# Kernel optimization log

Measured on AMD Instinct MI355X. Metric: run time of the kernel, lower is better.

The kernel has to match this reference:

```python
import jax, jax.numpy as jnp
import numpy as np

# dims
N = 10000      # nodes
E = 320000     # edges (avg degree 32)
NS = 64        # hidden 0e scalar channels
NV = 64        # hidden 1o vector channels
EMB = 32       # node-attr embedding dim
NTYPES = 20    # max_atom_types
NB = 8         # number_of_basis (bessel)
RH = 16        # radial_neurons
L = 2          # layers
CUT = 3.5      # max_radius
NNEIGH = 32.0  # num_neighbors normalization
H = 0.1        # residual step size


def smooth_cutoff(u):
    # e3nn example smooth_cutoff applied to x/max_radius
    v = 2.0 * (u - 1.0)
    y = 0.5 * (1.0 - jnp.cos(jnp.pi * v))
    y = jnp.where(v > 0.0, 0.0, y)
    y = jnp.where(v < -1.0, 1.0, y)
    return y


def setup_inputs() -> dict:
    key = jax.random.key(0)
    ks = jax.random.split(key, 10)
    x = jax.random.normal(ks[0], (N, 6), jnp.float32)
    batch = jnp.zeros((N,), jnp.int32)
    node_attr = jax.random.randint(ks[1], (N,), 0, NTYPES)
    edge_src = jax.random.randint(ks[2], (E,), 0, N)
    # avoid self-loops (zero edge length -> NaN in sh / bessel)
    off = jax.random.randint(ks[3], (E,), 1, N)
    edge_dst = (edge_src + off) % N
    embed_table = 0.1 * jax.random.normal(ks[4], (NTYPES, EMB), jnp.float32)
    Ku = jax.random.normal(ks[5], (2, NV), jnp.float32)          # uplift (made semi-unitary via QR)
    W_sc_s = 0.05 * jax.random.normal(ks[6], (L, NS, EMB, NS + NV), jnp.float32)  # self-connection TP: scalars
    W_sc_v = 0.05 * jax.random.normal(ks[7], (L, NV, EMB, NV), jnp.float32)       # self-connection TP: vectors
    Wr1 = 0.3 * jax.random.normal(ks[8], (L, NB, RH), jnp.float32)
    br1 = jnp.zeros((L, RH), jnp.float32)
    Wr2 = 0.3 * jax.random.normal(ks[9], (L, RH, 4 * NV), jnp.float32)
    br2 = jnp.zeros((L, 4 * NV), jnp.float32)
    return {"x": x, "batch": batch, "node_attr": node_attr, "edge_src": edge_src,
            "edge_dst": edge_dst, "embed_table": embed_table, "Ku": Ku,
            "W_sc_s": W_sc_s, "W_sc_v": W_sc_v, "Wr1": Wr1, "br1": br1,
            "Wr2": Wr2, "br2": br2}


def reference(x, batch, node_attr, edge_src, edge_dst, embed_table, Ku,
              W_sc_s, W_sc_v, Wr1, br1, Wr2, br2):
    n = x.shape[0]
    a = embed_table[node_attr]                     # [n, EMB] node-attr embedding (0e scalars)
    # make uplift semi-unitary: Q^T Q = I_2
    Q, _ = jnp.linalg.qr(Ku.T)                     # [NV, 2]
    U = Q.T                                        # uplift [2, NV]
    x_v = x.reshape(n, 2, 3)                       # 2x1o: position, velocity
    y_s = jnp.zeros((n, NS), x.dtype)              # uplift has no 1o->0e path
    y_v = jnp.einsum('ncd,ch->nhd', x_v, U)        # [n, NV, 3]
    nfreq = jnp.arange(1, NB + 1, dtype=x.dtype)
    inv_deg = 1.0 / np.sqrt(NNEIGH)
    for l in range(L):
        pos = x_v[:, 0, :]
        ev = pos[edge_src] - pos[edge_dst]                          # [E, 3]
        elen = jnp.linalg.norm(ev, axis=1)                          # [E]
        sh = jnp.sqrt(3.0) * ev / elen[:, None]                     # 1x1o SH, component norm
        # bessel radial basis, scaled by sqrt(NB)
        bess = (jnp.sqrt(2.0 / CUT) * jnp.sin(jnp.pi * nfreq * elen[:, None] / CUT)
                / elen[:, None]) * np.sqrt(NB)                      # [E, NB]
        ea = smooth_cutoff(elen / CUT)[:, None] * sh                # edge_attr [E, 3]
        # radial MLP -> per-edge tensor-product weights (4 paths x NV channels)
        w = jax.nn.silu(bess @ Wr1[l] + br1[l]) @ Wr2[l] + br2[l]   # [E, 4*NV]
        wA, wB, wC, wD = jnp.split(w, 4, axis=1)
        s_src = y_s[edge_src]                                       # [E, NS]
        v_src = y_v[edge_src]                                       # [E, NV, 3]
        # TP paths: 0e x 1o -> 1o ; 1o x 1o -> 1o (cross) ; 1o x 1o -> 0e (dot, feats + gates)
        msg_v = (wA[:, :, None] * s_src[:, :, None] * ea[:, None, :]
                 + wC[:, :, None] * jnp.cross(v_src, ea[:, None, :]))  # [E, NV, 3]
        dots = jnp.einsum('evd,ed->ev', v_src, ea)                  # [E, NV]
        msg_s = jnp.concatenate([wB * dots, wD * dots], axis=1)     # [E, NS+NV]
        agg_s = jax.ops.segment_sum(msg_s, edge_dst, num_segments=n) * inv_deg
        agg_v = (jax.ops.segment_sum(msg_v.reshape(msg_v.shape[0], -1), edge_dst,
                                     num_segments=n).reshape(n, NV, 3) * inv_deg)
        # self-connection: fully-connected TP with node-attr scalars
        sc_s = jnp.einsum('ns,ne,seo->no', y_s, a, W_sc_s[l])       # [n, NS+NV]
        sc_v = jnp.einsum('nvd,ne,veu->nud', y_v, a, W_sc_v[l])     # [n, NV, 3]
        out_s = sc_s + agg_s
        out_v = sc_v + agg_v
        # gate: silu on scalar feats, sigmoid gates scale the vectors
        y_s = y_s + H * jax.nn.silu(out_s[:, :NS])
        y_v = y_v + H * jax.nn.sigmoid(out_s[:, NS:])[:, :, None] * out_v
        # project back to 2x1o
        x_v = jnp.einsum('nhd,hc->ncd', y_v, Q)
    return x_v.reshape(n, 6)
```

## Files before the change

### kernel.cpp

```cpp
#include <hip/hip_runtime.h>
#include <math.h>

#define NSC 64
#define NVC 64
#define EMB 32
#define NTYPES 20
#define NB 8
#define RH 16
#define LAYERS 2
#define CUTV 3.5f
#define HSTEP 0.1f

__device__ __forceinline__ float wave_sum(float t)
{
  #pragma unroll
  for (int mm = 1; mm < 64; mm <<= 1) t += __shfl_xor(t, mm, 64);
  return t;
}

__global__ void qr_kernel(const float* __restrict__ Ku, float* __restrict__ Q)
{
  const int i = threadIdx.x;
  float a0 = Ku[i], a1 = Ku[64 + i];
  const float xn2 = wave_sum((i >= 1) ? a0 * a0 : 0.f);
  const float alpha = __shfl(a0, 0, 64);
  const float beta0 = -copysignf(sqrtf(alpha * alpha + xn2), alpha);
  const float tau0 = (beta0 - alpha) / beta0;
  const float inv0 = 1.f / (alpha - beta0);
  const float v0 = (i == 0) ? 1.f : a0 * inv0;
  const float w = wave_sum(v0 * a1);
  a1 -= tau0 * w * v0;
  const float alpha1 = __shfl(a1, 1, 64);
  const float xn2b = wave_sum((i >= 2) ? a1 * a1 : 0.f);
  const float beta1 = -copysignf(sqrtf(alpha1 * alpha1 + xn2b), alpha1);
  const float tau1 = (beta1 - alpha1) / beta1;
  const float inv1 = 1.f / (alpha1 - beta1);
  const float v1 = (i == 0) ? 0.f : ((i == 1) ? 1.f : a1 * inv1);
  const float t1v = ((i == 1) ? 1.f : 0.f) - tau1 * v1;
  const float d = wave_sum(v0 * t1v);
  Q[i * 2 + 0] = ((i == 0) ? 1.f : 0.f) - tau0 * v0;
  Q[i * 2 + 1] = t1v - tau0 * d * v0;
}

__global__ void init_state(const float* __restrict__ x, const float* __restrict__ Qm,
                           float4* __restrict__ st0, int* __restrict__ cnt, int n)
{
  const int i = blockIdx.x * 256 + threadIdx.x;
  const int node = i >> 6, lane = i & 63;
  if (node < n) {
    const float q0 = Qm[lane * 2 + 0], q1 = Qm[lane * 2 + 1];
    const float* xp = x + (size_t)node * 6;
    st0[i] = make_float4(0.f,
                         xp[0] * q0 + xp[3] * q1,
                         xp[1] * q0 + xp[4] * q1,
                         xp[2] * q0 + xp[5] * q1);
  }
  if (i < n) cnt[i] = 0;
}

__global__ void hist_kernel(const int* __restrict__ edst, int* __restrict__ cnt, int m)
{
  const int e = blockIdx.x * 256 + threadIdx.x;
  if (e < m) atomicAdd(&cnt[edst[e]], 1);
}

__global__ void scan_kernel(int* cnt, int* off, int n)
{
  __shared__ int lds[1024];
  const int t = threadIdx.x;
  const int CH = (n + 1023) >> 10;
  const int base = t * CH;
  int local[16];
  int run = 0;
  for (int j = 0; j < CH; ++j) {
    int v = (base + j < n) ? cnt[base + j] : 0;
    local[j] = run;
    run += v;
  }
  lds[t] = run;
  __syncthreads();
  for (int s = 1; s < 1024; s <<= 1) {
    int v = (t >= s) ? lds[t - s] : 0;
    __syncthreads();
    lds[t] += v;
    __syncthreads();
  }
  const int excl = lds[t] - run;
  for (int j = 0; j < CH; ++j) {
    if (base + j < n) {
      int o = excl + local[j];
      off[base + j] = o;
      cnt[base + j] = o;
    }
  }
  if (t == 1023) off[n] = lds[1023];
}

__global__ void scatter_kernel(const int* __restrict__ esrc, const int* __restrict__ edst,
                               int* __restrict__ cursor,
                               int* __restrict__ esrc_s, int* __restrict__ edst_s, int m)
{
  const int e = blockIdx.x * 256 + threadIdx.x;
  if (e < m) {
    const int d = edst[e];
    int p = atomicAdd(&cursor[d], 1);
    esrc_s[p] = esrc[e];
    edst_s[p] = d;
  }
}

__global__ void type_weights(const float* __restrict__ embed,
                             const float* __restrict__ Wss,
                             const float* __restrict__ Wsv,
                             float* __restrict__ Ws, float* __restrict__ Wv,
                             int total_s, int total_v)
{
  const int i = blockIdx.x * 256 + threadIdx.x;
  if (i < total_s) {
    const int bid = i >> 13;
    const int p = i & 8191;
    const int l = bid / NTYPES, t = bid % NTYPES;
    const int s = p >> 7, o = p & 127;
    const float* ar = embed + t * EMB;
    const float* wp = Wss + ((size_t)(l * 64 + s) * EMB) * 128 + o;
    float acc = 0.f;
    #pragma unroll
    for (int e = 0; e < EMB; ++e) acc = fmaf(ar[e], wp[e * 128], acc);
    Ws[i] = acc;
  } else {
    const int j = i - total_s;
    if (j < total_v) {
      const int bid = j >> 12;
      const int p = j & 4095;
      const int l = bid / NTYPES, t = bid % NTYPES;
      const int v = p >> 6, u = p & 63;
      const float* ar = embed + t * EMB;
      const float* wp = Wsv + ((size_t)(l * 64 + v) * EMB) * 64 + u;
      float acc = 0.f;
      #pragma unroll
      for (int e = 0; e < EMB; ++e) acc = fmaf(ar[e], wp[e * 64], acc);
      Wv[j] = acc;
    }
  }
}

__global__ void transpose_wr2(const float* __restrict__ Wr2, float* __restrict__ Wt)
{
  const int t = blockIdx.x * 256 + threadIdx.x;
  if (t >= LAYERS * 256) return;
  const int l = t >> 8, ch = t & 255;
  #pragma unroll
  for (int j = 0; j < RH; ++j)
    Wt[(size_t)l * 4096 + ch * RH + j] = Wr2[(size_t)l * 4096 + j * 256 + ch];
}

__global__ void edge_geom(const float* __restrict__ xv,
                          const int* __restrict__ esrc_s, const int* __restrict__ edst_s,
                          const float* __restrict__ Wr1l, const float* __restrict__ br1l,
                          float4* __restrict__ ea4, float* __restrict__ hidb, int m)
{
  const int k = blockIdx.x * 256 + threadIdx.x;
  if (k >= m) return;
  const int s = esrc_s[k], d = edst_s[k];
  const float ex = xv[(size_t)s * 6 + 0] - xv[(size_t)d * 6 + 0];
  const float ey = xv[(size_t)s * 6 + 1] - xv[(size_t)d * 6 + 1];
  const float ez = xv[(size_t)s * 6 + 2] - xv[(size_t)d * 6 + 2];
  const float len = sqrtf(ex * ex + ey * ey + ez * ez);
  const float invl = 1.f / len;
  const float u = len * (1.f / CUTV);
  const float arg = (float)M_PI * u;
  float sa, ca;
  __sincosf(arg, &sa, &ca);
  const float vv = 2.f * (u - 1.f);
  float cut = 0.5f * (1.f - (2.f * ca * ca - 1.f));
  cut = (vv > 0.f) ? 0.f : cut;
  cut = (vv < -1.f) ? 1.f : cut;
  const float cc = cut * 1.7320508075688772f * invl;
  ea4[k] = make_float4(cc * ex, cc * ey, cc * ez, 0.f);
  float bess[NB];
  const float amp = 2.1380899352993948f * invl;
  const float twoc = 2.f * ca;
  float sm1 = 0.f, scur = sa;
  #pragma unroll
  for (int kk = 0; kk < NB; ++kk) {
    bess[kk] = amp * scur;
    const float snext = twoc * scur - sm1;
    sm1 = scur; scur = snext;
  }
  float hid[RH];
  #pragma unroll
  for (int j = 0; j < RH; ++j) {
    float h = br1l[j];
    #pragma unroll
    for (int kk = 0; kk < NB; ++kk) h = fmaf(bess[kk], Wr1l[kk * RH + j], h);
    hid[j] = h / (1.f + expf(-h));
  }
  float4* hp = (float4*)(hidb + (size_t)k * 16);
  hp[0] = make_float4(hid[0],  hid[1],  hid[2],  hid[3]);
  hp[1] = make_float4(hid[4],  hid[5],  hid[6],  hid[7]);
  hp[2] = make_float4(hid[8],  hid[9],  hid[10], hid[11]);
  hp[3] = make_float4(hid[12], hid[13], hid[14], hid[15]);
}

#define MLPW                                                                  \
  float w = bias;                                                             \
  w = fmaf(g1.x, W0.x, w); w = fmaf(g1.y, W0.y, w);                           \
  w = fmaf(g1.z, W0.z, w); w = fmaf(g1.w, W0.w, w);                           \
  w = fmaf(g2.x, W1.x, w); w = fmaf(g2.y, W1.y, w);                           \
  w = fmaf(g2.z, W1.z, w); w = fmaf(g2.w, W1.w, w);                           \
  w = fmaf(g3.x, W2.x, w); w = fmaf(g3.y, W2.y, w);                           \
  w = fmaf(g3.z, W2.z, w); w = fmaf(g3.w, W2.w, w);                           \
  w = fmaf(g4.x, W3.x, w); w = fmaf(g4.y, W3.y, w);                           \
  w = fmaf(g4.z, W3.z, w); w = fmaf(g4.w, W3.w, w);

#define EDGE_PIPELINE(QSTMT)                                                  \
  {                                                                           \
    int k = k0;                                                               \
    for (; k + 4 <= k1; k += 4) {                                             \
      const int sA = esrc_s[k],     sB = esrc_s[k + 1];                       \
      const int sC = esrc_s[k + 2], sD = esrc_s[k + 3];                       \
      const float4 stA = st_in[(size_t)sA * 64 + lane];                       \
      const float4 stB = st_in[(size_t)sB * 64 + lane];                       \
      const float4 stC = st_in[(size_t)sC * 64 + lane];                       \
      const float4 stD = st_in[(size_t)sD * 64 + lane];                       \
      const float4 eaA = ea4[k],     eaB = ea4[k + 1];                        \
      const float4 eaC = ea4[k + 2], eaD = ea4[k + 3];                        \
      const float4* hb = (const float4*)(hidb + (size_t)k * 16);              \
      { const float4 g1 = hb[0], g2 = hb[1], g3 = hb[2], g4 = hb[3];          \
        const float4 stc = stA, ea = eaA; MLPW; QSTMT }                       \
      { const float4 g1 = hb[4], g2 = hb[5], g3 = hb[6], g4 = hb[7];          \
        const float4 stc = stB, ea = eaB; MLPW; QSTMT }                       \
      { const float4 g1 = hb[8], g2 = hb[9], g3 = hb[10], g4 = hb[11];        \
        const float4 stc = stC, ea = eaC; MLPW; QSTMT }                       \
      { const float4 g1 = hb[12], g2 = hb[13], g3 = hb[14], g4 = hb[15];      \
        const float4 stc = stD, ea = eaD; MLPW; QSTMT }                       \
    }                                                                         \
    for (; k < k1; ++k) {                                                     \
      const int sA = esrc_s[k];                                               \
      const float4 stc = st_in[(size_t)sA * 64 + lane];                       \
      const float4* hb = (const float4*)(hidb + (size_t)k * 16);              \
      const float4 g1 = hb[0], g2 = hb[1], g3 = hb[2], g4 = hb[3];            \
      const float4 ea = ea4[k];                                               \
      MLPW; QSTMT                                                             \
    }                                                                         \
  }

__global__ __launch_bounds__(256, 3) void gather_update(
    const int* __restrict__ off, const int* __restrict__ esrc_s,
    const float4* __restrict__ ea4, const float* __restrict__ hidb,
    const float4* __restrict__ st_in, const int* __restrict__ nattr,
    const float* __restrict__ Ws, const float* __restrict__ Wv,
    const float* __restrict__ Wtl, const float* __restrict__ br2l,
    const float* __restrict__ Qm,
    float4* __restrict__ st_out, float* __restrict__ xv_out, int n)
{
  __shared__ float eAx[64], eAy[64], eAz[64], eCx[64], eCy[64], eCz[64];
  __shared__ float eB[64], eD[64];
  __shared__ float oP[4][5][64];
  const int lane = threadIdx.x & 63;
  const int wid = threadIdx.x >> 6;
  const int node = blockIdx.x;

  const int chg = (wid << 6) + lane;
  const float* wp = Wtl + (size_t)chg * RH;
  const float4 W0 = *(const float4*)wp;
  const float4 W1 = *(const float4*)(wp + 4);
  const float4 W2 = *(const float4*)(wp + 8);
  const float4 W3 = *(const float4*)(wp + 12);
  const float bias = br2l[chg];

  float a0 = 0.f, a1 = 0.f, a2 = 0.f;
  const int k0 = off[node], k1 = off[node + 1];
  if (k0 < k1) {
    if (wid == 0) {
      EDGE_PIPELINE({
        const float t = w * stc.x;
        a0 = fmaf(t, ea.x, a0); a1 = fmaf(t, ea.y, a1); a2 = fmaf(t, ea.z, a2);
      })
    } else if (wid == 1) {
      EDGE_PIPELINE({
        const float dt = stc.y * ea.x + stc.z * ea.y + stc.w * ea.z;
        a0 = fmaf(w, dt, a0);
      })
    } else if (wid == 2) {
      EDGE_PIPELINE({
        a0 = fmaf(w, stc.z * ea.z - stc.w * ea.y, a0);
        a1 = fmaf(w, stc.w * ea.x - stc.y * ea.z, a1);
        a2 = fmaf(w, stc.y * ea.y - stc.z * ea.x, a2);
      })
    } else {
      EDGE_PIPELINE({
        const float dt = stc.y * ea.x + stc.z * ea.y + stc.w * ea.z;
        a0 = fmaf(w, dt, a0);
      })
    }
  }
  if (wid == 0)      { eAx[lane] = a0; eAy[lane] = a1; eAz[lane] = a2; }
  else if (wid == 1) { eB[lane] = a0; }
  else if (wid == 2) { eCx[lane] = a0; eCy[lane] = a1; eCz[lane] = a2; }
  else               { eD[lane] = a0; }

  const int ty = nattr[node];
  const float* WsT = Ws + (size_t)ty * 8192;
  const float* WvT = Wv + (size_t)ty * 4096;
  const float4 own = st_in[(size_t)node * 64 + lane];
  float oS1 = 0.f, oS2 = 0.f, oV0 = 0.f, oV1 = 0.f, oV2 = 0.f;
  const int s20 = wid << 4;
  #pragma unroll 4
  for (int s2 = s20; s2 < s20 + 16; ++s2) {
    const float yss = __shfl(own.x, s2, 64);
    const float b0 = __shfl(own.y, s2, 64);
    const float b1 = __shfl(own.z, s2, 64);
    const float b2 = __shfl(own.w, s2, 64);
    oS1 = fmaf(yss, WsT[s2 * 128 + lane], oS1);
    oS2 = fmaf(yss, WsT[s2 * 128 + 64 + lane], oS2);
    const float wvv = WvT[s2 * 64 + lane];
    oV0 = fmaf(b0, wvv, oV0);
    oV1 = fmaf(b1, wvv, oV1);
    oV2 = fmaf(b2, wvv, oV2);
  }
  oP[wid][0][lane] = oS1; oP[wid][1][lane] = oS2;
  oP[wid][2][lane] = oV0; oP[wid][3][lane] = oV1; oP[wid][4][lane] = oV2;
  __syncthreads();

  if (wid == 0) {
    const float inv_deg = 0.17677669529663687f;
    const float aS1 = eB[lane], aS2 = eD[lane];
    const float aV0 = eAx[lane] + eCx[lane];
    const float aV1 = eAy[lane] + eCy[lane];
    const float aV2 = eAz[lane] + eCz[lane];
    float s1 = 0.f, s2v = 0.f, v0 = 0.f, v1 = 0.f, v2 = 0.f;
    #pragma unroll
    for (int q = 0; q < 4; ++q) {
      s1 += oP[q][0][lane]; s2v += oP[q][1][lane];
      v0 += oP[q][2][lane]; v1 += oP[q][3][lane]; v2 += oP[q][4][lane];
    }
    const float outS1 = s1 + aS1 * inv_deg;
    const float outS2 = s2v + aS2 * inv_deg;
    const float sig1 = 1.f / (1.f + expf(-outS1));
    const float gate = 1.f / (1.f + expf(-outS2));
    const float ysn = own.x + HSTEP * outS1 * sig1;
    const float gf = HSTEP * gate;
    const float yvn0 = own.y + gf * (v0 + aV0 * inv_deg);
    const float yvn1 = own.z + gf * (v1 + aV1 * inv_deg);
    const float yvn2 = own.w + gf * (v2 + aV2 * inv_deg);
    st_out[(size_t)node * 64 + lane] = make_float4(ysn, yvn0, yvn1, yvn2);

    const float q0 = Qm[lane * 2 + 0], q1 = Qm[lane * 2 + 1];
    float pr[6] = { yvn0 * q0, yvn1 * q0, yvn2 * q0,
                    yvn0 * q1, yvn1 * q1, yvn2 * q1 };
    #pragma unroll
    for (int mm = 1; mm < 64; mm <<= 1) {
      #pragma unroll
      for (int i = 0; i < 6; ++i) pr[i] += __shfl_xor(pr[i], mm, 64);
    }
    if (lane == 0) {
      #pragma unroll
      for (int i = 0; i < 6; ++i) xv_out[(size_t)node * 6 + i] = pr[i];
    }
  }
}

extern "C" void kernel_launch(void* const* d_in, const int* in_sizes, int n_in,
                              void* d_out, int out_size, void* d_ws, size_t ws_size,
                              hipStream_t stream)
{
  const float* x     = (const float*)d_in[0];
  const int*   nattr = (const int*)d_in[2];
  const int*   esrc  = (const int*)d_in[3];
  const int*   edst  = (const int*)d_in[4];
  const float* embed = (const float*)d_in[5];
  const float* Ku    = (const float*)d_in[6];
  const float* Wss   = (const float*)d_in[7];
  const float* Wsv   = (const float*)d_in[8];
  const float* Wr1   = (const float*)d_in[9];
  const float* br1   = (const float*)d_in[10];
  const float* Wr2   = (const float*)d_in[11];
  const float* br2   = (const float*)d_in[12];
  const int n = in_sizes[0] / 6;
  const int m = in_sizes[3];

  char* p = (char*)d_ws;
  auto alloc = [&](size_t bytes) -> char* {
    char* r = p;
    p += (bytes + 255) & ~(size_t)255;
    return r;
  };
  int*    off    = (int*)alloc((size_t)(n + 1) * 4);
  int*    cursor = (int*)alloc((size_t)n * 4);
  int*    esrc_s = (int*)alloc((size_t)m * 4);
  int*    edst_s = (int*)alloc((size_t)m * 4);
  float*  Q      = (float*)alloc(128 * 4);
  float*  Ws     = (float*)alloc((size_t)LAYERS * NTYPES * 64 * 128 * 4);
  float*  Wv     = (float*)alloc((size_t)LAYERS * NTYPES * 64 * 64 * 4);
  float4* st0    = (float4*)alloc((size_t)n * 64 * 16);
  float4* st1    = (float4*)alloc((size_t)n * 64 * 16);
  float*  xvb    = (float*)alloc((size_t)n * 6 * 4);
  float4* ea4    = (float4*)alloc((size_t)m * 16);
  float*  hidb   = (float*)alloc((size_t)m * 16 * 4);
  float*  Wt     = (float*)alloc((size_t)LAYERS * 4096 * 4);

  const int total_s = LAYERS * NTYPES * 64 * 128;
  const int total_v = LAYERS * NTYPES * 64 * 64;

  qr_kernel<<<1, 64, 0, stream>>>(Ku, Q);
  init_state<<<(n * 64 + 255) / 256, 256, 0, stream>>>(x, Q, st0, cursor, n);
  hist_kernel<<<(m + 255) / 256, 256, 0, stream>>>(edst, cursor, m);
  scan_kernel<<<1, 1024, 0, stream>>>(cursor, off, n);
  scatter_kernel<<<(m + 255) / 256, 256, 0, stream>>>(esrc, edst, cursor, esrc_s, edst_s, m);
  type_weights<<<(total_s + total_v + 255) / 256, 256, 0, stream>>>(
      embed, Wss, Wsv, Ws, Wv, total_s, total_v);
  transpose_wr2<<<2, 256, 0, stream>>>(Wr2, Wt);

  const float* xv_cur = x;
  const float4* st_cur = st0;
  float4* st_nxt = st1;
  for (int l = 0; l < LAYERS; ++l) {
    edge_geom<<<(m + 255) / 256, 256, 0, stream>>>(
        xv_cur, esrc_s, edst_s, Wr1 + l * NB * RH, br1 + l * RH, ea4, hidb, m);
    float* xv_out = (l == LAYERS - 1) ? (float*)d_out : xvb;
    gather_update<<<n, 256, 0, stream>>>(
        off, esrc_s, ea4, hidb, st_cur, nattr,
        Ws + (size_t)l * NTYPES * 8192, Wv + (size_t)l * NTYPES * 4096,
        Wt + (size_t)l * 4096, br2 + l * 256, Q,
        st_nxt, xv_out, n);
    xv_cur = xv_out;
    float4* ts = (float4*)st_cur; st_cur = st_nxt; st_nxt = ts;
  }
}
```

Baseline: 305.4 us.

## Share gathered source rows across waves via double-buffered LDS staging

Each of the four waves used to gather every neighbour's 1 KB source-node row from global memory on its own. Now each wave loads two of every eight edges into a double-buffered shared-memory stage, and all waves read from it. The next batch's loads are issued before the current batch is consumed. This cuts redundant global gathers by roughly fourfold, at the cost of 16 KB more LDS per block (possibly lower occupancy), a block-wide barrier per 8-edge batch, and masked padding work on partial batches.

```diff
diff --git a/kernel.cpp b/kernel.cpp
--- a/kernel.cpp
+++ b/kernel.cpp
@@ -213,36 +213,19 @@
   w = fmaf(g4.x, W3.x, w); w = fmaf(g4.y, W3.y, w);                           \
   w = fmaf(g4.z, W3.z, w); w = fmaf(g4.w, W3.w, w);
 
-#define EDGE_PIPELINE(QSTMT)                                                  \
-  {                                                                           \
-    int k = k0;                                                               \
-    for (; k + 4 <= k1; k += 4) {                                             \
-      const int sA = esrc_s[k],     sB = esrc_s[k + 1];                       \
-      const int sC = esrc_s[k + 2], sD = esrc_s[k + 3];                       \
-      const float4 stA = st_in[(size_t)sA * 64 + lane];                       \
-      const float4 stB = st_in[(size_t)sB * 64 + lane];                       \
-      const float4 stC = st_in[(size_t)sC * 64 + lane];                       \
-      const float4 stD = st_in[(size_t)sD * 64 + lane];                       \
-      const float4 eaA = ea4[k],     eaB = ea4[k + 1];                        \
-      const float4 eaC = ea4[k + 2], eaD = ea4[k + 3];                        \
-      const float4* hb = (const float4*)(hidb + (size_t)k * 16);              \
-      { const float4 g1 = hb[0], g2 = hb[1], g3 = hb[2], g4 = hb[3];          \
-        const float4 stc = stA, ea = eaA; MLPW; QSTMT }                       \
-      { const float4 g1 = hb[4], g2 = hb[5], g3 = hb[6], g4 = hb[7];          \
-        const float4 stc = stB, ea = eaB; MLPW; QSTMT }                       \
-      { const float4 g1 = hb[8], g2 = hb[9], g3 = hb[10], g4 = hb[11];        \
-        const float4 stc = stC, ea = eaC; MLPW; QSTMT }                       \
-      { const float4 g1 = hb[12], g2 = hb[13], g3 = hb[14], g4 = hb[15];      \
-        const float4 stc = stD, ea = eaD; MLPW; QSTMT }                       \
-    }                                                                         \
-    for (; k < k1; ++k) {                                                     \
-      const int sA = esrc_s[k];                                               \
-      const float4 stc = st_in[(size_t)sA * 64 + lane];                       \
-      const float4* hb = (const float4*)(hidb + (size_t)k * 16);              \
-      const float4 g1 = hb[0], g2 = hb[1], g3 = hb[2], g4 = hb[3];            \
-      const float4 ea = ea4[k];                                               \
-      MLPW; QSTMT                                                             \
-    }                                                                         \
+#define CONSUME(QSTMT)                                                        \
+  _Pragma("unroll")                                                           \
+  for (int e = 0; e < 8; ++e) {                                               \
+    const int kk = kb + e;                                                    \
+    const int idx = (kk < k1) ? kk : (k1 - 1);                                \
+    const float mval = (kk < k1) ? 1.f : 0.f;                                 \
+    const float4 stc = stg[cur][e][lane];                                     \
+    const float4* hb = (const float4*)(hidb + (size_t)idx * 16);              \
+    const float4 g1 = hb[0], g2 = hb[1], g3 = hb[2], g4 = hb[3];              \
+    const float4 ea = ea4[idx];                                               \
+    MLPW;                                                                     \
+    w *= mval;                                                                \
+    QSTMT                                                                     \
   }
 
 __global__ __launch_bounds__(256, 3) void gather_update(
@@ -254,6 +237,7 @@
     const float* __restrict__ Qm,
     float4* __restrict__ st_out, float* __restrict__ xv_out, int n)
 {
+  __shared__ float4 stg[2][8][64];
   __shared__ float eAx[64], eAy[64], eAz[64], eCx[64], eCy[64], eCz[64];
   __shared__ float eB[64], eD[64];
   __shared__ float oP[4][5][64];
@@ -272,27 +256,57 @@
   float a0 = 0.f, a1 = 0.f, a2 = 0.f;
   const int k0 = off[node], k1 = off[node + 1];
   if (k0 < k1) {
-    if (wid == 0) {
-      EDGE_PIPELINE({
-        const float t = w * stc.x;
-        a0 = fmaf(t, ea.x, a0); a1 = fmaf(t, ea.y, a1); a2 = fmaf(t, ea.z, a2);
-      })
-    } else if (wid == 1) {
-      EDGE_PIPELINE({
-        const float dt = stc.y * ea.x + stc.z * ea.y + stc.w * ea.z;
-        a0 = fmaf(w, dt, a0);
-      })
-    } else if (wid == 2) {
-      EDGE_PIPELINE({
-        a0 = fmaf(w, stc.z * ea.z - stc.w * ea.y, a0);
-        a1 = fmaf(w, stc.w * ea.x - stc.y * ea.z, a1);
-        a2 = fmaf(w, stc.y * ea.y - stc.z * ea.x, a2);
-      })
-    } else {
-      EDGE_PIPELINE({
-        const float dt = stc.y * ea.x + stc.z * ea.y + stc.w * ea.z;
-        a0 = fmaf(w, dt, a0);
-      })
+    const int nb = (k1 - k0 + 7) >> 3;
+    {
+      const int i0 = k0 + wid, i1 = k0 + 4 + wid;
+      const int s0 = esrc_s[(i0 < k1) ? i0 : (k1 - 1)];
+      const int s1 = esrc_s[(i1 < k1) ? i1 : (k1 - 1)];
+      const float4 r0 = st_in[(size_t)s0 * 64 + lane];
+      const float4 r1 = st_in[(size_t)s1 * 64 + lane];
+      stg[0][wid][lane] = r0;
+      stg[0][wid + 4][lane] = r1;
+    }
+    __syncthreads();
+    for (int b = 0; b < nb; ++b) {
+      const int kb = k0 + (b << 3);
+      const int cur = b & 1, nxt = cur ^ 1;
+      float4 r0, r1;
+      const bool have_next = (b + 1 < nb);
+      if (have_next) {
+        const int kn = kb + 8;
+        const int i0 = kn + wid, i1 = kn + 4 + wid;
+        const int s0 = esrc_s[(i0 < k1) ? i0 : (k1 - 1)];
+        const int s1 = esrc_s[(i1 < k1) ? i1 : (k1 - 1)];
+        r0 = st_in[(size_t)s0 * 64 + lane];
+        r1 = st_in[(size_t)s1 * 64 + lane];
+      }
+      if (wid == 0) {
+        CONSUME({
+          const float t = w * stc.x;
+          a0 = fmaf(t, ea.x, a0); a1 = fmaf(t, ea.y, a1); a2 = fmaf(t, ea.z, a2);
+        })
+      } else if (wid == 1) {
+        CONSUME({
+          const float dt = stc.y * ea.x + stc.z * ea.y + stc.w * ea.z;
+          a0 = fmaf(w, dt, a0);
+        })
+      } else if (wid == 2) {
+        CONSUME({
+          a0 = fmaf(w, stc.z * ea.z - stc.w * ea.y, a0);
+          a1 = fmaf(w, stc.w * ea.x - stc.y * ea.z, a1);
+          a2 = fmaf(w, stc.y * ea.y - stc.z * ea.x, a2);
+        })
+      } else {
+        CONSUME({
+          const float dt = stc.y * ea.x + stc.z * ea.y + stc.w * ea.z;
+          a0 = fmaf(w, dt, a0);
+        })
+      }
+      if (have_next) {
+        stg[nxt][wid][lane] = r0;
+        stg[nxt][wid + 4][lane] = r1;
+      }
+      __syncthreads();
     }
   }
   if (wid == 0)      { eAx[lane] = a0; eAy[lane] = a1; eAz[lane] = a2; }
```

Measured after the change: 383.2 us. +25.5%, slower.

## Store node state in bf16 and gather 8 edges per masked batch

Applied to the files above, without the earlier changes.

Node state (scalar plus vector channels) is now stored as bf16 ushort4 instead of float4, which halves the bytes of the random per-edge gathers of source-node state in gather_update. The edge loop now fetches 8 edges per iteration with clamped indices and a zero mask on padded slots, replacing the 4-wide loop plus scalar tail, to keep more loads in flight. The cost is reduced precision in the state carried between layers, extra register pressure, and wasted work on padded edges.

```diff
diff --git a/kernel.cpp b/kernel.cpp
--- a/kernel.cpp
+++ b/kernel.cpp
@@ -10,6 +10,17 @@
 #define LAYERS 2
 #define CUTV 3.5f
 #define HSTEP 0.1f
+
+__device__ __forceinline__ unsigned short f2bf(float f)
+{
+  unsigned u = __float_as_uint(f);
+  unsigned r = (u + 0x7FFFu + ((u >> 16) & 1u)) >> 16;
+  return (unsigned short)r;
+}
+__device__ __forceinline__ float bf2f(unsigned short u)
+{
+  return __uint_as_float(((unsigned)u) << 16);
+}
 
 __device__ __forceinline__ float wave_sum(float t)
 {
@@ -43,17 +54,17 @@
 }
 
 __global__ void init_state(const float* __restrict__ x, const float* __restrict__ Qm,
-                           float4* __restrict__ st0, int* __restrict__ cnt, int n)
+                           ushort4* __restrict__ st0, int* __restrict__ cnt, int n)
 {
   const int i = blockIdx.x * 256 + threadIdx.x;
   const int node = i >> 6, lane = i & 63;
   if (node < n) {
     const float q0 = Qm[lane * 2 + 0], q1 = Qm[lane * 2 + 1];
     const float* xp = x + (size_t)node * 6;
-    st0[i] = make_float4(0.f,
-                         xp[0] * q0 + xp[3] * q1,
-                         xp[1] * q0 + xp[4] * q1,
-                         xp[2] * q0 + xp[5] * q1);
+    st0[i] = make_ushort4(0,
+                          f2bf(xp[0] * q0 + xp[3] * q1),
+                          f2bf(xp[1] * q0 + xp[4] * q1),
+                          f2bf(xp[2] * q0 + xp[5] * q1));
   }
   if (i < n) cnt[i] = 0;
 }
@@ -214,45 +225,42 @@
   w = fmaf(g4.z, W3.z, w); w = fmaf(g4.w, W3.w, w);
 
 #define EDGE_PIPELINE(QSTMT)                                                  \
-  {                                                                           \
-    int k = k0;                                                               \
-    for (; k + 4 <= k1; k += 4) {                                             \
-      const int sA = esrc_s[k],     sB = esrc_s[k + 1];                       \
-      const int sC = esrc_s[k + 2], sD = esrc_s[k + 3];                       \
-      const float4 stA = st_in[(size_t)sA * 64 + lane];                       \
-      const float4 stB = st_in[(size_t)sB * 64 + lane];                       \
-      const float4 stC = st_in[(size_t)sC * 64 + lane];                       \
-      const float4 stD = st_in[(size_t)sD * 64 + lane];                       \
-      const float4 eaA = ea4[k],     eaB = ea4[k + 1];                        \
-      const float4 eaC = ea4[k + 2], eaD = ea4[k + 3];                        \
-      const float4* hb = (const float4*)(hidb + (size_t)k * 16);              \
-      { const float4 g1 = hb[0], g2 = hb[1], g3 = hb[2], g4 = hb[3];          \
-        const float4 stc = stA, ea = eaA; MLPW; QSTMT }                       \
-      { const float4 g1 = hb[4], g2 = hb[5], g3 = hb[6], g4 = hb[7];          \
-        const float4 stc = stB, ea = eaB; MLPW; QSTMT }                       \
-      { const float4 g1 = hb[8], g2 = hb[9], g3 = hb[10], g4 = hb[11];        \
-        const float4 stc = stC, ea = eaC; MLPW; QSTMT }                       \
-      { const float4 g1 = hb[12], g2 = hb[13], g3 = hb[14], g4 = hb[15];      \
-        const float4 stc = stD, ea = eaD; MLPW; QSTMT }                       \
+  for (int k = k0; k < k1; k += 8) {                                          \
+    int idx[8];                                                               \
+    float msk[8];                                                             \
+    _Pragma("unroll")                                                         \
+    for (int j = 0; j < 8; ++j) {                                             \
+      idx[j] = (k + j < k1) ? (k + j) : (k1 - 1);                             \
+      msk[j] = (k + j < k1) ? 1.f : 0.f;                                      \
     }                                                                         \
-    for (; k < k1; ++k) {                                                     \
-      const int sA = esrc_s[k];                                               \
-      const float4 stc = st_in[(size_t)sA * 64 + lane];                       \
-      const float4* hb = (const float4*)(hidb + (size_t)k * 16);              \
+    ushort4 stP[8];                                                           \
+    _Pragma("unroll")                                                         \
+    for (int j = 0; j < 8; ++j)                                               \
+      stP[j] = st_in[(size_t)esrc_s[idx[j]] * 64 + lane];                     \
+    float4 eaP[8];                                                            \
+    _Pragma("unroll")                                                         \
+    for (int j = 0; j < 8; ++j) eaP[j] = ea4[idx[j]];                         \
+    _Pragma("unroll")                                                         \
+    for (int j = 0; j < 8; ++j) {                                             \
+      const float4* hb = (const float4*)(hidb + (size_t)idx[j] * 16);         \
       const float4 g1 = hb[0], g2 = hb[1], g3 = hb[2], g4 = hb[3];            \
-      const float4 ea = ea4[k];                                               \
-      MLPW; QSTMT                                                             \
+      const float4 stc = make_float4(bf2f(stP[j].x), bf2f(stP[j].y),          \
+                                     bf2f(stP[j].z), bf2f(stP[j].w));         \
+      const float4 ea = eaP[j];                                               \
+      MLPW;                                                                   \
+      w *= msk[j];                                                            \
+      QSTMT                                                                   \
     }                                                                         \
   }
 
 __global__ __launch_bounds__(256, 3) void gather_update(
     const int* __restrict__ off, const int* __restrict__ esrc_s,
     const float4* __restrict__ ea4, const float* __restrict__ hidb,
-    const float4* __restrict__ st_in, const int* __restrict__ nattr,
+    const ushort4* __restrict__ st_in, const int* __restrict__ nattr,
     const float* __restrict__ Ws, const float* __restrict__ Wv,
     const float* __restrict__ Wtl, const float* __restrict__ br2l,
     const float* __restrict__ Qm,
-    float4* __restrict__ st_out, float* __restrict__ xv_out, int n)
+    ushort4* __restrict__ st_out, float* __restrict__ xv_out, int n)
 {
   __shared__ float eAx[64], eAy[64], eAz[64], eCx[64], eCy[64], eCz[64];
   __shared__ float eB[64], eD[64];
@@ -303,15 +311,17 @@
   const int ty = nattr[node];
   const float* WsT = Ws + (size_t)ty * 8192;
   const float* WvT = Wv + (size_t)ty * 4096;
-  const float4 own = st_in[(size_t)node * 64 + lane];
+  const ushort4 ownb = st_in[(size_t)node * 64 + lane];
+  const float own_s = bf2f(ownb.x), own_x = bf2f(ownb.y),
+              own_y = bf2f(ownb.z), own_z = bf2f(ownb.w);
   float oS1 = 0.f, oS2 = 0.f, oV0 = 0.f, oV1 = 0.f, oV2 = 0.f;
   const int s20 = wid << 4;
   #pragma unroll 4
   for (int s2 = s20; s2 < s20 + 16; ++s2) {
-    const float yss = __shfl(own.x, s2, 64);
-    const float b0 = __shfl(own.y, s2, 64);
-    const float b1 = __shfl(own.z, s2, 64);
-    const float b2 = __shfl(own.w, s2, 64);
+    const float yss = __shfl(own_s, s2, 64);
+    const float b0 = __shfl(own_x, s2, 64);
+    const float b1 = __shfl(own_y, s2, 64);
+    const float b2 = __shfl(own_z, s2, 64);
     oS1 = fmaf(yss, WsT[s2 * 128 + lane], oS1);
     oS2 = fmaf(yss, WsT[s2 * 128 + 64 + lane], oS2);
     const float wvv = WvT[s2 * 64 + lane];
@@ -339,12 +349,13 @@
     const float outS2 = s2v + aS2 * inv_deg;
     const float sig1 = 1.f / (1.f + expf(-outS1));
     const float gate = 1.f / (1.f + expf(-outS2));
-    const float ysn = own.x + HSTEP * outS1 * sig1;
+    const float ysn = own_s + HSTEP * outS1 * sig1;
     const float gf = HSTEP * gate;
-    const float yvn0 = own.y + gf * (v0 + aV0 * inv_deg);
-    const float yvn1 = own.z + gf * (v1 + aV1 * inv_deg);
-    const float yvn2 = own.w + gf * (v2 + aV2 * inv_deg);
-    st_out[(size_t)node * 64 + lane] = make_float4(ysn, yvn0, yvn1, yvn2);
+    const float yvn0 = own_x + gf * (v0 + aV0 * inv_deg);
+    const float yvn1 = own_y + gf * (v1 + aV1 * inv_deg);
+    const float yvn2 = own_z + gf * (v2 + aV2 * inv_deg);
+    st_out[(size_t)node * 64 + lane] =
+        make_ushort4(f2bf(ysn), f2bf(yvn0), f2bf(yvn1), f2bf(yvn2));
 
     const float q0 = Qm[lane * 2 + 0], q1 = Qm[lane * 2 + 1];
     float pr[6] = { yvn0 * q0, yvn1 * q0, yvn2 * q0,
@@ -386,19 +397,19 @@
     p += (bytes + 255) & ~(size_t)255;
     return r;
   };
-  int*    off    = (int*)alloc((size_t)(n + 1) * 4);
-  int*    cursor = (int*)alloc((size_t)n * 4);
-  int*    esrc_s = (int*)alloc((size_t)m * 4);
-  int*    edst_s = (int*)alloc((size_t)m * 4);
-  float*  Q      = (float*)alloc(128 * 4);
-  float*  Ws     = (float*)alloc((size_t)LAYERS * NTYPES * 64 * 128 * 4);
-  float*  Wv     = (float*)alloc((size_t)LAYERS * NTYPES * 64 * 64 * 4);
-  float4* st0    = (float4*)alloc((size_t)n * 64 * 16);
-  float4* st1    = (float4*)alloc((size_t)n * 64 * 16);
-  float*  xvb    = (float*)alloc((size_t)n * 6 * 4);
-  float4* ea4    = (float4*)alloc((size_t)m * 16);
-  float*  hidb   = (float*)alloc((size_t)m * 16 * 4);
-  float*  Wt     = (float*)alloc((size_t)LAYERS * 4096 * 4);
+  int*     off    = (int*)alloc((size_t)(n + 1) * 4);
+  int*     cursor = (int*)alloc((size_t)n * 4);
+  int*     esrc_s = (int*)alloc((size_t)m * 4);
+  int*     edst_s = (int*)alloc((size_t)m * 4);
+  float*   Q      = (float*)alloc(128 * 4);
+  float*   Ws     = (float*)alloc((size_t)LAYERS * NTYPES * 64 * 128 * 4);
+  float*   Wv     = (float*)alloc((size_t)LAYERS * NTYPES * 64 * 64 * 4);
+  ushort4* st0    = (ushort4*)alloc((size_t)n * 64 * 8);
+  ushort4* st1    = (ushort4*)alloc((size_t)n * 64 * 8);
+  float*   xvb    = (float*)alloc((size_t)n * 6 * 4);
+  float4*  ea4    = (float4*)alloc((size_t)m * 16);
+  float*   hidb   = (float*)alloc((size_t)m * 16 * 4);
+  float*   Wt     = (float*)alloc((size_t)LAYERS * 4096 * 4);
 
   const int total_s = LAYERS * NTYPES * 64 * 128;
   const int total_v = LAYERS * NTYPES * 64 * 64;
@@ -413,8 +424,8 @@
   transpose_wr2<<<2, 256, 0, stream>>>(Wr2, Wt);
 
   const float* xv_cur = x;
-  const float4* st_cur = st0;
-  float4* st_nxt = st1;
+  const ushort4* st_cur = st0;
+  ushort4* st_nxt = st1;
   for (int l = 0; l < LAYERS; ++l) {
     edge_geom<<<(m + 255) / 256, 256, 0, stream>>>(
         xv_cur, esrc_s, edst_s, Wr1 + l * NB * RH, br1 + l * RH, ea4, hidb, m);
@@ -425,6 +436,6 @@
         Wt + (size_t)l * 4096, br2 + l * 256, Q,
         st_nxt, xv_out, n);
     xv_cur = xv_out;
-    float4* ts = (float4*)st_cur; st_cur = st_nxt; st_nxt = ts;
-  }
-}
+    ushort4* ts = (ushort4*)st_cur; st_cur = st_nxt; st_nxt = ts;
+  }
+}
```

Measured after the change: 320.5 us. 1.05x slower.
